# Kernel optimization log

Hardware: AMD Instinct MI355X
Metric: run time of the kernel (lower is better)

The kernel has to match this reference:

```python
import jax, jax.numpy as jnp
import numpy as np

EPS_NORM = 1e-12  # matches F.normalize eps

def _l2_normalize(x):
    norm = jnp.sqrt(jnp.sum(x * x, axis=-1, keepdims=True))
    return x / jnp.maximum(norm, EPS_NORM)

def setup_inputs() -> dict:
    key = jax.random.key(0)
    k1, k2 = jax.random.split(key)
    N, C, D = 16384, 8192, 1024
    features = jax.random.normal(k1, (N, D), dtype=jnp.float32)
    # prototypes init: normal(mean=const_init=0, std=0.01)
    prototypes = 0.01 * jax.random.normal(k2, (C, D), dtype=jnp.float32)
    distance_scale = jnp.ones((1,), dtype=jnp.float32)
    return {"features": features, "prototypes": prototypes, "distance_scale": distance_scale}

def reference(features, prototypes, distance_scale):
    temperature = 1.0
    f = _l2_normalize(features)      # [N, D]
    p = _l2_normalize(prototypes)    # [C, D]
    # Both rows are unit-norm, so ||f_i - p_j||^2 = 2 - 2 f_i . p_j
    dots = jnp.einsum('nd,cd->nc', f, p)             # [N, C]
    sq = jnp.maximum(2.0 - 2.0 * dots, 1e-12)
    distances = jnp.abs(distance_scale[0]) * jnp.sqrt(sq)
    logits = -distances
    return logits / temperature
```

## Files before the change

kernel.cpp:

```cpp
#include <hip/hip_runtime.h>
#include <hip/hip_bf16.h>
#include <stdint.h>

using bf16x8 = __attribute__((ext_vector_type(8))) short;
using f32x4  = __attribute__((ext_vector_type(4))) float;

__device__ __forceinline__ void gload_lds16(const void* g, void* l) {
  __builtin_amdgcn_global_load_lds(
      (const __attribute__((address_space(1))) void*)g,
      (__attribute__((address_space(3))) void*)l,
      16, 0, 0);
}

__device__ __forceinline__ short f2bf(float f) {
  union { float f; uint32_t u; } c; c.f = f;
  uint32_t u = c.u;
  uint32_t r = (u + 0x7fffu + ((u >> 16) & 1u)) >> 16;
  return (short)(r & 0xffffu);
}

__global__ __launch_bounds__(256) void norm_rows(
    const float* __restrict__ F, const float* __restrict__ P,
    short* __restrict__ Fb, short* __restrict__ Pb, int nF) {
  int row = blockIdx.x;
  const float* src; short* dst;
  if (row < nF) {
    src = F + (size_t)row * 1024; dst = Fb + (size_t)row * 1024;
  } else {
    int r = row - nF;
    src = P + (size_t)r * 1024; dst = Pb + (size_t)r * 1024;
  }
  int tid = threadIdx.x;
  float4 v = ((const float4*)src)[tid];
  float ss = v.x * v.x + v.y * v.y + v.z * v.z + v.w * v.w;
  #pragma unroll
  for (int off = 32; off >= 1; off >>= 1) ss += __shfl_xor(ss, off);
  __shared__ float wsum[4];
  if ((tid & 63) == 0) wsum[tid >> 6] = ss;
  __syncthreads();
  float tot = wsum[0] + wsum[1] + wsum[2] + wsum[3];
  float inv = 1.0f / fmaxf(sqrtf(tot), 1e-12f);
  short4 o;
  o.x = f2bf(v.x * inv); o.y = f2bf(v.y * inv);
  o.z = f2bf(v.z * inv); o.w = f2bf(v.w * inv);
  ((short4*)dst)[tid] = o;
}

#define BM 128
#define BN 128
#define BK 32

__global__ __launch_bounds__(256) void gemm_epi(
    const short* __restrict__ A,
    const short* __restrict__ B,
    const float* __restrict__ scale,
    float* __restrict__ Out, int M, int Cc, int K) {
  __shared__ __align__(16) short As[BM * BK];
  __shared__ __align__(16) short Bs[BN * BK];

  const int tid  = threadIdx.x;
  const int wave = tid >> 6;
  const int lane = tid & 63;

  const int nwg = gridDim.x;
  const int cpx = nwg >> 3;
  const int bid = blockIdx.x;
  const int swz = (bid & 7) * cpx + (bid >> 3);
  const int ntn = Cc / BN;
  const int tm = swz / ntn;
  const int tn = swz % ntn;

  const short* Abase = A + (size_t)tm * BM * K;
  const short* Bbase = B + (size_t)tn * BN * K;

  const int srow = wave * 32 + (lane >> 2);
  const int scol = (lane & 3) * 8;

  const int wr = wave >> 1, wc = wave & 1;
  const int fr = lane & 15;
  const int fk = (lane >> 4) * 8;

  f32x4 acc[4][4];
  #pragma unroll
  for (int i = 0; i < 4; ++i)
    #pragma unroll
    for (int j = 0; j < 4; ++j)
      acc[i][j] = (f32x4){0.f, 0.f, 0.f, 0.f};

  for (int k0 = 0; k0 < K; k0 += BK) {
    const short* ag = Abase + (size_t)srow * K + k0 + scol;
    const short* bg = Bbase + (size_t)srow * K + k0 + scol;
    gload_lds16(ag,          &As[(wave * 32) * BK]);
    gload_lds16(ag + 16 * K, &As[(wave * 32 + 16) * BK]);
    gload_lds16(bg,          &Bs[(wave * 32) * BK]);
    gload_lds16(bg + 16 * K, &Bs[(wave * 32 + 16) * BK]);
    __syncthreads();

    bf16x8 af[4], bfr[4];
    #pragma unroll
    for (int mi = 0; mi < 4; ++mi)
      af[mi] = *(const bf16x8*)&As[(wr * 64 + mi * 16 + fr) * BK + fk];
    #pragma unroll
    for (int ni = 0; ni < 4; ++ni)
      bfr[ni] = *(const bf16x8*)&Bs[(wc * 64 + ni * 16 + fr) * BK + fk];
    #pragma unroll
    for (int mi = 0; mi < 4; ++mi)
      #pragma unroll
      for (int ni = 0; ni < 4; ++ni)
        acc[mi][ni] = __builtin_amdgcn_mfma_f32_16x16x32_bf16(
            af[mi], bfr[ni], acc[mi][ni], 0, 0, 0);
    __syncthreads();
  }

  const float s = fabsf(scale[0]);
  const int col0  = tn * BN + wc * 64 + (lane & 15);
  const int row00 = tm * BM + wr * 64 + (lane >> 4) * 4;
  #pragma unroll
  for (int mi = 0; mi < 4; ++mi) {
    #pragma unroll
    for (int ni = 0; ni < 4; ++ni) {
      f32x4 a = acc[mi][ni];
      const int col = col0 + ni * 16;
      #pragma unroll
      for (int r = 0; r < 4; ++r) {
        float d  = a[r];
        float sq = fmaxf(2.0f - 2.0f * d, 1e-12f);
        Out[(size_t)(row00 + mi * 16 + r) * Cc + col] = -s * sqrtf(sq);
      }
    }
  }
}

extern "C" void kernel_launch(void* const* d_in, const int* in_sizes, int n_in,
                              void* d_out, int out_size, void* d_ws, size_t ws_size,
                              hipStream_t stream) {
  const float* F = (const float*)d_in[0];
  const float* P = (const float*)d_in[1];
  const float* S = (const float*)d_in[2];
  float* Out = (float*)d_out;

  const int D = 1024;
  const int N = in_sizes[0] / D;
  const int C = in_sizes[1] / D;

  short* Fb = (short*)d_ws;
  short* Pb = Fb + (size_t)N * D;

  norm_rows<<<N + C, 256, 0, stream>>>(F, P, Fb, Pb, N);

  dim3 grid((N / BM) * (C / BN));
  gemm_epi<<<grid, 256, 0, stream>>>(Fb, Pb, S, Out, N, C, D);
}
```

Baseline: 927.3 us.

## Rewrite GEMM with 256x256x64 tiles, double-buffered LDS, swizzled layout, phased MFMA schedule

The GEMM moves from 128x128x32 tiles with 4 waves to 256x256x64 tiles with 8 waves. Each wave now computes a 128x64 sub-tile, and global-to-LDS loads are double-buffered so the next K-slice prefetches while the current one computes. The LDS layout uses an XOR swizzle to cut bank conflicts. The inner loop is split into four phases using sched barriers, setprio and explicit waitcnts to interleave LDS reads with MFMA, and output uses nontemporal stores. This targets low arithmetic intensity and exposed load latency, at the cost of 128KB LDS per block and higher register pressure that may limit occupancy.

After: 845.4 us. -8.8%, faster.

```diff
diff --git a/kernel.cpp b/kernel.cpp
--- a/kernel.cpp
+++ b/kernel.cpp
@@ -4,6 +4,11 @@
 
 using bf16x8 = __attribute__((ext_vector_type(8))) short;
 using f32x4  = __attribute__((ext_vector_type(4))) float;
+
+#define SBAR()   __builtin_amdgcn_s_barrier()
+#define SCHED0() __builtin_amdgcn_sched_barrier(0)
+#define LGKM0()  asm volatile("s_waitcnt lgkmcnt(0)" ::: "memory")
+#define VM0()    asm volatile("s_waitcnt vmcnt(0)" ::: "memory")
 
 __device__ __forceinline__ void gload_lds16(const void* g, void* l) {
   __builtin_amdgcn_global_load_lds(
@@ -46,89 +51,163 @@
   ((short4*)dst)[tid] = o;
 }
 
-#define BM 128
-#define BN 128
-#define BK 32
-
-__global__ __launch_bounds__(256) void gemm_epi(
+#define BM 256
+#define BN 256
+#define BK 64
+
+__global__ __launch_bounds__(512, 2) void gemm_epi(
     const short* __restrict__ A,
     const short* __restrict__ B,
     const float* __restrict__ scale,
     float* __restrict__ Out, int M, int Cc, int K) {
-  __shared__ __align__(16) short As[BM * BK];
-  __shared__ __align__(16) short Bs[BN * BK];
+  __shared__ __align__(16) char smem[2 * 65536];
 
   const int tid  = threadIdx.x;
   const int wave = tid >> 6;
   const int lane = tid & 63;
+  const int wm = wave >> 2;
+  const int wn = wave & 3;
+  const int hb = wn >> 1;
+  const int rbB = (wn & 1) * 4;
 
   const int nwg = gridDim.x;
   const int cpx = nwg >> 3;
-  const int bid = blockIdx.x;
-  const int swz = (bid & 7) * cpx + (bid >> 3);
+  const int swz = (blockIdx.x & 7) * cpx + (blockIdx.x >> 3);
   const int ntn = Cc / BN;
-  const int tm = swz / ntn;
-  const int tn = swz % ntn;
-
-  const short* Abase = A + (size_t)tm * BM * K;
-  const short* Bbase = B + (size_t)tn * BN * K;
-
-  const int srow = wave * 32 + (lane >> 2);
-  const int scol = (lane & 3) * 8;
-
-  const int wr = wave >> 1, wc = wave & 1;
-  const int fr = lane & 15;
-  const int fk = (lane >> 4) * 8;
-
-  f32x4 acc[4][4];
+  const int tm = swz / ntn, tn = swz % ntn;
+
+  const size_t Kb = (size_t)K * 2;
+  const char* Ag = (const char*)A + (size_t)tm * BM * Kb;
+  const char* Bg = (const char*)B + (size_t)tn * BN * Kb;
+
+  int r0, c0, r1, c1;
+  { int s = tid * 16;        int st = s >> 10, w = s & 1023;
+    w ^= ((w >> 9) & 1) << 5; r0 = ((st >> 1) << 4) + (w >> 6); c0 = ((st & 1) << 6) + (w & 63); }
+  { int s = 8192 + tid * 16; int st = s >> 10, w = s & 1023;
+    w ^= ((w >> 9) & 1) << 5; r1 = ((st >> 1) << 4) + (w >> 6); c1 = ((st & 1) << 6) + (w & 63); }
+
+  const int fr  = lane & 15;
+  const int fk2 = ((lane >> 4) * 8) * 2;
+  const int fragoff = fr * 64 + (fk2 ^ ((fr & 8) ? 32 : 0));
+
+  const char* smA = smem + wm * 16384;
+  const char* smB = smem + 32768 + hb * 16384;
+
+  f32x4 acc[8][4];
   #pragma unroll
-  for (int i = 0; i < 4; ++i)
-    #pragma unroll
-    for (int j = 0; j < 4; ++j)
-      acc[i][j] = (f32x4){0.f, 0.f, 0.f, 0.f};
-
-  for (int k0 = 0; k0 < K; k0 += BK) {
-    const short* ag = Abase + (size_t)srow * K + k0 + scol;
-    const short* bg = Bbase + (size_t)srow * K + k0 + scol;
-    gload_lds16(ag,          &As[(wave * 32) * BK]);
-    gload_lds16(ag + 16 * K, &As[(wave * 32 + 16) * BK]);
-    gload_lds16(bg,          &Bs[(wave * 32) * BK]);
-    gload_lds16(bg + 16 * K, &Bs[(wave * 32 + 16) * BK]);
-    __syncthreads();
-
-    bf16x8 af[4], bfr[4];
-    #pragma unroll
-    for (int mi = 0; mi < 4; ++mi)
-      af[mi] = *(const bf16x8*)&As[(wr * 64 + mi * 16 + fr) * BK + fk];
-    #pragma unroll
-    for (int ni = 0; ni < 4; ++ni)
-      bfr[ni] = *(const bf16x8*)&Bs[(wc * 64 + ni * 16 + fr) * BK + fk];
-    #pragma unroll
-    for (int mi = 0; mi < 4; ++mi)
-      #pragma unroll
-      for (int ni = 0; ni < 4; ++ni)
-        acc[mi][ni] = __builtin_amdgcn_mfma_f32_16x16x32_bf16(
-            af[mi], bfr[ni], acc[mi][ni], 0, 0, 0);
-    __syncthreads();
+  for (int i = 0; i < 8; ++i)
+    #pragma unroll
+    for (int j = 0; j < 4; ++j) acc[i][j] = (f32x4){0.f, 0.f, 0.f, 0.f};
+
+  const int nt = K / BK;
+
+  #define STAGE(t, buf) do {                                                   \
+    const size_t kb = (size_t)(t) * (BK * 2);                                  \
+    char* db = smem + (buf) * 65536 + wave * 1024;                             \
+    gload_lds16(Ag + (size_t)(      r0) * Kb + kb + c0, db);                   \
+    gload_lds16(Ag + (size_t)(      r1) * Kb + kb + c1, db + 8192);            \
+    gload_lds16(Ag + (size_t)(128 + r0) * Kb + kb + c0, db + 16384);           \
+    gload_lds16(Ag + (size_t)(128 + r1) * Kb + kb + c1, db + 16384 + 8192);    \
+    gload_lds16(Bg + (size_t)(      r0) * Kb + kb + c0, db + 32768);           \
+    gload_lds16(Bg + (size_t)(      r1) * Kb + kb + c1, db + 32768 + 8192);    \
+    gload_lds16(Bg + (size_t)(128 + r0) * Kb + kb + c0, db + 49152);           \
+    gload_lds16(Bg + (size_t)(128 + r1) * Kb + kb + c1, db + 49152 + 8192);    \
+  } while (0)
+
+  #define LDA(buf, mi, ks) (*(const bf16x8*)(smA + (buf) * 65536 + ((mi) * 2 + (ks)) * 1024 + fragoff))
+  #define LDB(buf, ni, ks) (*(const bf16x8*)(smB + (buf) * 65536 + ((rbB + (ni)) * 2 + (ks)) * 1024 + fragoff))
+
+  STAGE(0, 0);
+  VM0(); SCHED0(); SBAR(); SCHED0();
+
+  for (int t = 0; t < nt; ++t) {
+    const int cur = t & 1, nxt = cur ^ 1;
+    if (t + 1 < nt) STAGE(t + 1, nxt);
+
+    bf16x8 a03[4][2], b01[2][2];
+    #pragma unroll
+    for (int mi = 0; mi < 4; ++mi) { a03[mi][0] = LDA(cur, mi, 0); a03[mi][1] = LDA(cur, mi, 1); }
+    #pragma unroll
+    for (int ni = 0; ni < 2; ++ni) { b01[ni][0] = LDB(cur, ni, 0); b01[ni][1] = LDB(cur, ni, 1); }
+    SBAR(); LGKM0(); SCHED0();
+    __builtin_amdgcn_s_setprio(1);
+    #pragma unroll
+    for (int mi = 0; mi < 4; ++mi)
+      #pragma unroll
+      for (int ni = 0; ni < 2; ++ni) {
+        acc[mi][ni] = __builtin_amdgcn_mfma_f32_16x16x32_bf16(a03[mi][0], b01[ni][0], acc[mi][ni], 0, 0, 0);
+        acc[mi][ni] = __builtin_amdgcn_mfma_f32_16x16x32_bf16(a03[mi][1], b01[ni][1], acc[mi][ni], 0, 0, 0);
+      }
+    __builtin_amdgcn_s_setprio(0);
+    SBAR(); SCHED0();
+
+    bf16x8 b23[2][2];
+    #pragma unroll
+    for (int ni = 0; ni < 2; ++ni) { b23[ni][0] = LDB(cur, 2 + ni, 0); b23[ni][1] = LDB(cur, 2 + ni, 1); }
+    SBAR(); LGKM0(); SCHED0();
+    __builtin_amdgcn_s_setprio(1);
+    #pragma unroll
+    for (int mi = 0; mi < 4; ++mi)
+      #pragma unroll
+      for (int ni = 0; ni < 2; ++ni) {
+        acc[mi][2 + ni] = __builtin_amdgcn_mfma_f32_16x16x32_bf16(a03[mi][0], b23[ni][0], acc[mi][2 + ni], 0, 0, 0);
+        acc[mi][2 + ni] = __builtin_amdgcn_mfma_f32_16x16x32_bf16(a03[mi][1], b23[ni][1], acc[mi][2 + ni], 0, 0, 0);
+      }
+    __builtin_amdgcn_s_setprio(0);
+    SBAR(); SCHED0();
+
+    bf16x8 a47[4][2];
+    #pragma unroll
+    for (int mi = 0; mi < 4; ++mi) { a47[mi][0] = LDA(cur, 4 + mi, 0); a47[mi][1] = LDA(cur, 4 + mi, 1); }
+    SBAR(); LGKM0(); SCHED0();
+    __builtin_amdgcn_s_setprio(1);
+    #pragma unroll
+    for (int mi = 0; mi < 4; ++mi)
+      #pragma unroll
+      for (int ni = 0; ni < 2; ++ni) {
+        acc[4 + mi][2 + ni] = __builtin_amdgcn_mfma_f32_16x16x32_bf16(a47[mi][0], b23[ni][0], acc[4 + mi][2 + ni], 0, 0, 0);
+        acc[4 + mi][2 + ni] = __builtin_amdgcn_mfma_f32_16x16x32_bf16(a47[mi][1], b23[ni][1], acc[4 + mi][2 + ni], 0, 0, 0);
+      }
+    __builtin_amdgcn_s_setprio(0);
+    SBAR(); SCHED0();
+
+    bf16x8 b01b[2][2];
+    #pragma unroll
+    for (int ni = 0; ni < 2; ++ni) { b01b[ni][0] = LDB(cur, ni, 0); b01b[ni][1] = LDB(cur, ni, 1); }
+    SBAR(); LGKM0(); SCHED0();
+    __builtin_amdgcn_s_setprio(1);
+    #pragma unroll
+    for (int mi = 0; mi < 4; ++mi)
+      #pragma unroll
+      for (int ni = 0; ni < 2; ++ni) {
+        acc[4 + mi][ni] = __builtin_amdgcn_mfma_f32_16x16x32_bf16(a47[mi][0], b01b[ni][0], acc[4 + mi][ni], 0, 0, 0);
+        acc[4 + mi][ni] = __builtin_amdgcn_mfma_f32_16x16x32_bf16(a47[mi][1], b01b[ni][1], acc[4 + mi][ni], 0, 0, 0);
+      }
+    __builtin_amdgcn_s_setprio(0);
+    VM0(); SCHED0();
+    SBAR(); SCHED0();
   }
 
-  const float s = fabsf(scale[0]);
-  const int col0  = tn * BN + wc * 64 + (lane & 15);
-  const int row00 = tm * BM + wr * 64 + (lane >> 4) * 4;
+  const float sc = fabsf(scale[0]);
+  const int orow0 = tm * BM + wm * 128 + (lane >> 4) * 4;
+  const int ocol0 = tn * BN + wn * 64 + fr;
   #pragma unroll
-  for (int mi = 0; mi < 4; ++mi) {
+  for (int mi = 0; mi < 8; ++mi) {
     #pragma unroll
     for (int ni = 0; ni < 4; ++ni) {
-      f32x4 a = acc[mi][ni];
-      const int col = col0 + ni * 16;
+      const int col = ocol0 + ni * 16;
       #pragma unroll
       for (int r = 0; r < 4; ++r) {
-        float d  = a[r];
+        float d  = acc[mi][ni][r];
         float sq = fmaxf(2.0f - 2.0f * d, 1e-12f);
-        Out[(size_t)(row00 + mi * 16 + r) * Cc + col] = -s * sqrtf(sq);
+        __builtin_nontemporal_store(-sc * sqrtf(sq),
+            &Out[(size_t)(orow0 + mi * 16 + r) * Cc + col]);
       }
     }
   }
+  #undef STAGE
+  #undef LDA
+  #undef LDB
 }
 
 extern "C" void kernel_launch(void* const* d_in, const int* in_sizes, int n_in,
@@ -149,5 +228,5 @@
   norm_rows<<<N + C, 256, 0, stream>>>(F, P, Fb, Pb, N);
 
   dim3 grid((N / BM) * (C / BN));
-  gemm_epi<<<grid, 256, 0, stream>>>(Fb, Pb, S, Out, N, C, D);
-}
+  gemm_epi<<<grid, 512, 0, stream>>>(Fb, Pb, S, Out, N, C, D);
+}
```
